# Kernel tuning notes

Measured on AMD Instinct MI355X. Metric: run time of the kernel, lower is better.

## Reference

```python
import jax, jax.numpy as jnp
import numpy as np

PLP_ORDER = 16
N_CHANNEL = 40
FFT_LENGTH = 512
SAMPLE_RATE = 16000
LIFTER = 22
COMP_FACTOR = 0.33
FLOOR = 1e-5
F_MIN = 0.0
F_MAX = SAMPLE_RATE / 2


def _hz_to_mel(hz):
    return 1127.0 * np.log1p(np.asarray(hz, dtype=np.float64) / 700.0)


def _mel_to_hz(mel):
    return 700.0 * np.expm1(np.asarray(mel, dtype=np.float64) / 1127.0)


def _build_constants():
    # SPTK-style mel filter bank (triangular in mel domain).
    mel_min = _hz_to_mel(F_MIN)
    mel_max = _hz_to_mel(F_MAX)
    lower_bin = max(1, int(F_MIN / SAMPLE_RATE * FFT_LENGTH + 1.5))
    upper_bin = min(FFT_LENGTH // 2, int(F_MAX / SAMPLE_RATE * FFT_LENGTH + 0.5))
    seed = np.arange(1, N_CHANNEL + 2)
    cf_mel = (mel_max - mel_min) / (N_CHANNEL + 1) * seed + mel_min  # (C+1,)
    bins = np.arange(lower_bin, upper_bin)
    mel = _hz_to_mel(SAMPLE_RATE * bins / FFT_LENGTH)
    ch = np.searchsorted(cf_mel, mel, side='left')  # first center freq >= mel
    diff = cf_mel - np.concatenate([[mel_min], cf_mel[:-1]])
    w = (cf_mel[ch] - mel) / diff[ch]
    H = np.zeros((len(bins), N_CHANNEL))
    rows = np.arange(len(bins))
    low = ch - 1
    m_lo = low >= 0
    H[rows[m_lo], low[m_lo]] += w[m_lo]
    m_hi = ch <= N_CHANNEL - 1
    H[rows[m_hi], ch[m_hi]] += 1.0 - w[m_hi]
    # Equal-loudness curve over the first C center frequencies (in Hz).
    cf_hz = _mel_to_hz(cf_mel)
    f2 = cf_hz[:N_CHANNEL] ** 2
    eql = (f2 / (f2 + 160000.0)) ** 2 * (f2 + 1440000.0) / (f2 + 9610000.0)
    # Liftering vector, v[0] = 2.
    m = np.arange(PLP_ORDER + 1)
    lift = 1.0 + LIFTER / 2.0 * np.sin(np.pi / LIFTER * m)
    lift[0] = 2.0
    return lower_bin, upper_bin, H.astype(np.float32), eql.astype(np.float32), lift.astype(np.float32)


LOWER_BIN, UPPER_BIN, H_NP, EQL_NP, LIFT_NP = _build_constants()


def _levinson_durbin(r):
    # r: (..., M+1) autocorrelation -> (gain K, LPC coefficients a_1..a_M)
    M = PLP_ORDER
    E = r[..., 0]
    a = jnp.zeros(r.shape[:-1] + (M,), r.dtype)
    for i in range(1, M + 1):
        acc = r[..., i]
        if i > 1:
            acc = acc + jnp.einsum('...j,...j->...', a[..., : i - 1], r[..., 1:i][..., ::-1])
        k = -acc / E
        if i > 1:
            a = a.at[..., : i - 1].set(a[..., : i - 1] + k[..., None] * a[..., : i - 1][..., ::-1])
        a = a.at[..., i - 1].set(k)
        E = E * (1.0 - k * k)
    return jnp.sqrt(E), a


def _lpc_to_cepstrum(K, a):
    # c0 = log K; c_m = -a_m - sum_{k=1}^{m-1} (k/m) c_k a_{m-k}
    M = PLP_ORDER
    c = [jnp.log(K)]
    for m in range(1, M + 1):
        acc = a[..., m - 1]
        for k in range(1, m):
            acc = acc + (k / m) * c[k] * a[..., m - k - 1]
        c.append(-acc)
    return jnp.stack(c, axis=-1)  # (..., M+1)


def _plp(x):
    H = jnp.asarray(H_NP)
    eql = jnp.asarray(EQL_NP)
    lift = jnp.asarray(LIFT_NP)
    # Mel filter bank on power spectrum (use_power=True)
    fb = jnp.matmul(x[..., LOWER_BIN:UPPER_BIN], H)          # (..., C)
    logfb = jnp.log(jnp.maximum(fb, FLOOR))
    # Equal-loudness scaling + cubic-root amplitude compression
    y = (jnp.exp(logfb) * eql) ** COMP_FACTOR                # (..., C)
    # replicate1: duplicate first and last channels
    y = jnp.concatenate([y[..., :1], y, y[..., -1:]], axis=-1)  # (..., C+2)
    n = y.shape[-1]
    # hfft with norm='forward' -> inverse-FFT-like autocorrelation
    r = jnp.fft.hfft(y) / (2 * (n - 1))
    r = r[..., : PLP_ORDER + 1]
    K, a = _levinson_durbin(r)
    c = _lpc_to_cepstrum(K, a)
    c = c * lift
    return c[..., 1:]  # out_format 'y': PLP without C0, (..., M)


def setup_inputs() -> dict:
    key = jax.random.key(0)
    x = jax.random.uniform(key, (32, 4096, FFT_LENGTH // 2 + 1), dtype=jnp.float32)
    return {"x": x}


def reference(x):
    return _plp(x)
```

## Files before the change

### kernel.cpp

```cpp
#include <hip/hip_runtime.h>
#include <cmath>

#define NBINS 257
#define NCH   40
#define MORD  16
#define NR    17
#define NY    42
#define CHUNK 16
#define FPB   64

__global__ __launch_bounds__(256) void plp_kernel(const float* __restrict__ x,
                                                  float* __restrict__ out,
                                                  int nframes)
{
    __shared__ float xs[CHUNK][257];
    __shared__ float ys[CHUNK][NY + 1];
    __shared__ float rs[FPB][NR];
    __shared__ float ttab[256];
    __shared__ int   sstart[NCH + 2];
    __shared__ float eql_s[NCH];
    __shared__ float lift_s[NR];
    __shared__ float ct[NR][NY + 1];

    const int tid = threadIdx.x;
    const double PI = 3.14159265358979323846;

    const double MELMAX = 1127.0 * log1p(8000.0 / 700.0);
    const double U = MELMAX / 41.0;
    if (tid < 255) {
        int b = tid + 1;
        double mel = 1127.0 * log1p((31.25 * (double)b) / 700.0);
        ttab[b] = (float)(mel / U);
    }
    if (tid < NCH + 2) {
        double thr = 22.4 * expm1(((double)tid * U) / 1127.0);
        int s = (int)floor(thr) + 1;
        s = s < 1 ? 1 : (s > 256 ? 256 : s);
        sstart[tid] = s;
    }
    if (tid < NCH) {
        double cf = 700.0 * expm1(((double)(tid + 1) * U) / 1127.0);
        double f2 = cf * cf;
        double e  = f2 / (f2 + 160000.0);
        e = e * e * (f2 + 1440000.0) / (f2 + 9610000.0);
        eql_s[tid] = (float)e;
    }
    if (tid < NR) {
        lift_s[tid] = (float)(1.0 + 11.0 * sin(PI * (double)tid / 22.0));
    }
    for (int idx = tid; idx < NR * NY; idx += 256) {
        int l = idx / NY, j = idx % NY;
        double s = (j == 0 || j == NY - 1) ? 1.0 : 2.0;
        ct[l][j] = (float)(s * cos(PI * (double)(j * l) / 41.0) / 82.0);
    }
    __syncthreads();

    const long long frame0 = (long long)blockIdx.x * FPB;

    for (int chk = 0; chk < FPB / CHUNK; ++chk) {
        const long long cf0 = frame0 + (long long)chk * CHUNK;

        #pragma unroll
        for (int i = 0; i < CHUNK; ++i) {
            long long fr = cf0 + i;
            if (fr > (long long)nframes - 1) fr = (long long)nframes - 1;
            xs[i][tid] = x[fr * NBINS + 1 + tid];
        }
        __syncthreads();

        for (int task = tid; task < CHUNK * NCH; task += 256) {
            int f = task / NCH, c = task % NCH;
            int s0 = sstart[c], s1 = sstart[c + 1], s2 = sstart[c + 2];
            float acc = 0.f;
            for (int b = s0; b < s1; ++b) acc = fmaf(ttab[b] - (float)c, xs[f][b - 1], acc);
            for (int b = s1; b < s2; ++b) acc = fmaf((float)(c + 2) - ttab[b], xs[f][b - 1], acc);
            float v  = fmaxf(acc, 1e-5f) * eql_s[c];
            float yv = powf(v, 0.33f);
            ys[f][c + 1] = yv;
            if (c == 0)       ys[f][0]      = yv;
            if (c == NCH - 1) ys[f][NY - 1] = yv;
        }
        __syncthreads();

        for (int task = tid; task < CHUNK * NR; task += 256) {
            int f = task / NR, l = task % NR;
            float acc = 0.f;
            #pragma unroll
            for (int j = 0; j < NY; ++j) acc = fmaf(ct[l][j], ys[f][j], acc);
            rs[chk * CHUNK + f][l] = acc;
        }
        __syncthreads();
    }

    if (tid < FPB && frame0 + tid < (long long)nframes) {
        float r[NR];
        #pragma unroll
        for (int i = 0; i < NR; ++i) r[i] = rs[tid][i];

        float a[MORD];
        #pragma unroll
        for (int i = 0; i < MORD; ++i) a[i] = 0.f;
        float E = r[0];
        #pragma unroll
        for (int i = 1; i <= MORD; ++i) {
            float acc = r[i];
            #pragma unroll
            for (int j = 0; j < i - 1; ++j) acc = fmaf(a[j], r[i - 1 - j], acc);
            float k = -acc / E;
            const int half = (i - 1) / 2;
            #pragma unroll
            for (int j = 0; j < half; ++j) {
                float t1 = a[j], t2 = a[i - 2 - j];
                a[j]         = fmaf(k, t2, t1);
                a[i - 2 - j] = fmaf(k, t1, t2);
            }
            if ((i - 1) & 1) {
                a[half] = fmaf(k, a[half], a[half]);
            }
            a[i - 1] = k;
            E = E * (1.f - k * k);
        }

        float cc[NR];
        #pragma unroll
        for (int m = 1; m <= MORD; ++m) {
            float acc = a[m - 1];
            #pragma unroll
            for (int k2 = 1; k2 < m; ++k2)
                acc = fmaf(((float)k2 / (float)m) * cc[k2], a[m - k2 - 1], acc);
            cc[m] = -acc;
        }

        float o[16];
        #pragma unroll
        for (int m = 1; m <= MORD; ++m) o[m - 1] = cc[m] * lift_s[m];

        float4* op = reinterpret_cast<float4*>(out + (size_t)(frame0 + tid) * 16);
        op[0] = make_float4(o[0],  o[1],  o[2],  o[3]);
        op[1] = make_float4(o[4],  o[5],  o[6],  o[7]);
        op[2] = make_float4(o[8],  o[9],  o[10], o[11]);
        op[3] = make_float4(o[12], o[13], o[14], o[15]);
    }
}

extern "C" void kernel_launch(void* const* d_in, const int* in_sizes, int n_in,
                              void* d_out, int out_size, void* d_ws, size_t ws_size,
                              hipStream_t stream) {
    const float* x  = (const float*)d_in[0];
    float*      outp = (float*)d_out;
    int nframes = in_sizes[0] / NBINS;
    int nblocks = (nframes + FPB - 1) / FPB;
    plp_kernel<<<nblocks, 256, 0, stream>>>(x, outp, nframes);
}
```

Baseline: 239.7 us.

## Compute each frame entirely per thread with compile-time constant tables

Replaces the block-cooperative shared-memory pipeline with a one-thread-per-frame kernel. All filterbank weights, DCT cosines, equal-loudness and lifter tables are computed at compile time via constexpr, so they become immediates and the per-block table setup and barriers disappear. powf is swapped for fast exp/log intrinsics. The risk is uncoalesced strided global loads, since each thread reads its own 257-float row, plus heavy register pressure from the fully unrolled per-thread state.

```diff
diff --git a/kernel.cpp b/kernel.cpp
--- a/kernel.cpp
+++ b/kernel.cpp
@@ -1,154 +1,180 @@
 #include <hip/hip_runtime.h>
-#include <cmath>
 
-#define NBINS 257
 #define NCH   40
 #define MORD  16
 #define NR    17
 #define NY    42
-#define CHUNK 16
-#define FPB   64
+#define NBINS 257
+
+namespace cfg {
+
+constexpr double PI  = 3.14159265358979323846264338327950288;
+constexpr double LN2 = 0.693147180559945309417232121458176568;
+
+constexpr double cexp(double x) {
+    double t = 1.0, s = 1.0;
+    for (int i = 1; i < 40; ++i) { t *= x / i; s += t; }
+    return s;
+}
+
+constexpr double clog(double z) {
+    double lg = 0.0;
+    while (z > 1.4142135623730951) { z *= 0.5; lg += LN2; }
+    while (z < 0.7071067811865476) { z *= 2.0; lg -= LN2; }
+    double u = (z - 1.0) / (z + 1.0), u2 = u * u, t = u, s = u;
+    for (int k = 1; k < 24; ++k) { t *= u2; s += t / (2.0 * k + 1.0); }
+    return lg + 2.0 * s;
+}
+
+constexpr double ccos(double x) {
+    double tp = 2.0 * PI;
+    double q = x / tp;
+    long long k = (long long)(q + (q >= 0.0 ? 0.5 : -0.5));
+    double r = x - (double)k * tp;
+    double r2 = r * r, t = 1.0, s = 1.0;
+    for (int i = 1; i < 20; ++i) { t *= -r2 / ((2.0 * i - 1.0) * (2.0 * i)); s += t; }
+    return s;
+}
+
+constexpr double csin(double x) { return ccos(x - PI / 2.0); }
+
+struct Tab {
+    int   start[43];
+    float w[257];
+    float eql[NCH];
+    float lift[NR];
+    float ct[NR][NY];
+    constexpr Tab() : start(), w(), eql(), lift(), ct() {
+        const double lmax  = clog(87.0 / 7.0);
+        const double U1127 = lmax / 41.0;
+        for (int c = 0; c <= 42 - 1; ++c) {
+            double thr = 22.4 * (cexp((double)c * U1127) - 1.0);
+            int s = (int)thr + 1;
+            if (s < 1) s = 1;
+            if (s > 256) s = 256;
+            start[c] = s;
+        }
+        start[42 - 1] = start[41];
+        for (int c = 0; c <= 40; ++c) {
+            for (int b = start[c]; b < start[c + 1]; ++b) {
+                double mel = 1127.0 * clog(1.0 + (double)b * 31.25 / 700.0);
+                double t   = mel / (1127.0 * U1127);
+                w[b] = (float)(t - (double)c);
+            }
+        }
+        for (int c = 0; c < NCH; ++c) {
+            double cf = 700.0 * (cexp((double)(c + 1) * U1127) - 1.0);
+            double f2 = cf * cf;
+            double e  = f2 / (f2 + 160000.0);
+            e = e * e * (f2 + 1440000.0) / (f2 + 9610000.0);
+            eql[c] = (float)e;
+        }
+        for (int m = 0; m < NR; ++m)
+            lift[m] = (float)(1.0 + 11.0 * csin(PI * (double)m / 22.0));
+        lift[0] = 2.0f;
+        for (int l = 0; l < NR; ++l)
+            for (int j = 0; j < NY; ++j) {
+                double s = (j == 0 || j == NY - 1) ? 1.0 : 2.0;
+                ct[l][j] = (float)(s * ccos(PI * (double)(j * l) / 41.0) / 82.0);
+            }
+    }
+};
+
+constexpr Tab T{};
+
+}
 
 __global__ __launch_bounds__(256) void plp_kernel(const float* __restrict__ x,
                                                   float* __restrict__ out,
                                                   int nframes)
 {
-    __shared__ float xs[CHUNK][257];
-    __shared__ float ys[CHUNK][NY + 1];
-    __shared__ float rs[FPB][NR];
-    __shared__ float ttab[256];
-    __shared__ int   sstart[NCH + 2];
-    __shared__ float eql_s[NCH];
-    __shared__ float lift_s[NR];
-    __shared__ float ct[NR][NY + 1];
+    using cfg::T;
+    const long long frame = (long long)blockIdx.x * blockDim.x + threadIdx.x;
+    if (frame >= nframes) return;
+    const float* __restrict__ xf = x + frame * NBINS;
 
-    const int tid = threadIdx.x;
-    const double PI = 3.14159265358979323846;
+    float fb[NCH];
+    #pragma unroll
+    for (int c = 0; c < NCH; ++c) fb[c] = 0.f;
 
-    const double MELMAX = 1127.0 * log1p(8000.0 / 700.0);
-    const double U = MELMAX / 41.0;
-    if (tid < 255) {
-        int b = tid + 1;
-        double mel = 1127.0 * log1p((31.25 * (double)b) / 700.0);
-        ttab[b] = (float)(mel / U);
-    }
-    if (tid < NCH + 2) {
-        double thr = 22.4 * expm1(((double)tid * U) / 1127.0);
-        int s = (int)floor(thr) + 1;
-        s = s < 1 ? 1 : (s > 256 ? 256 : s);
-        sstart[tid] = s;
-    }
-    if (tid < NCH) {
-        double cf = 700.0 * expm1(((double)(tid + 1) * U) / 1127.0);
-        double f2 = cf * cf;
-        double e  = f2 / (f2 + 160000.0);
-        e = e * e * (f2 + 1440000.0) / (f2 + 9610000.0);
-        eql_s[tid] = (float)e;
-    }
-    if (tid < NR) {
-        lift_s[tid] = (float)(1.0 + 11.0 * sin(PI * (double)tid / 22.0));
-    }
-    for (int idx = tid; idx < NR * NY; idx += 256) {
-        int l = idx / NY, j = idx % NY;
-        double s = (j == 0 || j == NY - 1) ? 1.0 : 2.0;
-        ct[l][j] = (float)(s * cos(PI * (double)(j * l) / 41.0) / 82.0);
-    }
-    __syncthreads();
-
-    const long long frame0 = (long long)blockIdx.x * FPB;
-
-    for (int chk = 0; chk < FPB / CHUNK; ++chk) {
-        const long long cf0 = frame0 + (long long)chk * CHUNK;
-
+    #pragma unroll
+    for (int c = 0; c <= 40; ++c) {
         #pragma unroll
-        for (int i = 0; i < CHUNK; ++i) {
-            long long fr = cf0 + i;
-            if (fr > (long long)nframes - 1) fr = (long long)nframes - 1;
-            xs[i][tid] = x[fr * NBINS + 1 + tid];
+        for (int b = T.start[c]; b < T.start[c + 1]; ++b) {
+            float xv = xf[b];
+            const float wa = T.w[b];
+            if (c < 40) fb[c]     = fmaf(wa, xv, fb[c]);
+            if (c >= 1) fb[c - 1] = fmaf(1.0f - wa, xv, fb[c - 1]);
         }
-        __syncthreads();
-
-        for (int task = tid; task < CHUNK * NCH; task += 256) {
-            int f = task / NCH, c = task % NCH;
-            int s0 = sstart[c], s1 = sstart[c + 1], s2 = sstart[c + 2];
-            float acc = 0.f;
-            for (int b = s0; b < s1; ++b) acc = fmaf(ttab[b] - (float)c, xs[f][b - 1], acc);
-            for (int b = s1; b < s2; ++b) acc = fmaf((float)(c + 2) - ttab[b], xs[f][b - 1], acc);
-            float v  = fmaxf(acc, 1e-5f) * eql_s[c];
-            float yv = powf(v, 0.33f);
-            ys[f][c + 1] = yv;
-            if (c == 0)       ys[f][0]      = yv;
-            if (c == NCH - 1) ys[f][NY - 1] = yv;
-        }
-        __syncthreads();
-
-        for (int task = tid; task < CHUNK * NR; task += 256) {
-            int f = task / NR, l = task % NR;
-            float acc = 0.f;
-            #pragma unroll
-            for (int j = 0; j < NY; ++j) acc = fmaf(ct[l][j], ys[f][j], acc);
-            rs[chk * CHUNK + f][l] = acc;
-        }
-        __syncthreads();
     }
 
-    if (tid < FPB && frame0 + tid < (long long)nframes) {
-        float r[NR];
+    float ys[NY];
+    #pragma unroll
+    for (int c = 0; c < NCH; ++c) {
+        float v = fmaxf(fb[c], 1e-5f) * T.eql[c];
+        ys[c + 1] = __expf(0.33f * __logf(v));
+    }
+    ys[0] = ys[1];
+    ys[NY - 1] = ys[NY - 2];
+
+    float r[NR];
+    #pragma unroll
+    for (int l = 0; l < NR; ++l) {
+        float acc = 0.f;
         #pragma unroll
-        for (int i = 0; i < NR; ++i) r[i] = rs[tid][i];
+        for (int j = 0; j < NY; ++j) acc = fmaf(T.ct[l][j], ys[j], acc);
+        r[l] = acc;
+    }
 
-        float a[MORD];
+    float a[MORD];
+    #pragma unroll
+    for (int i = 0; i < MORD; ++i) a[i] = 0.f;
+    float E = r[0];
+    #pragma unroll
+    for (int i = 1; i <= MORD; ++i) {
+        float acc = r[i];
         #pragma unroll
-        for (int i = 0; i < MORD; ++i) a[i] = 0.f;
-        float E = r[0];
+        for (int j = 0; j < i - 1; ++j) acc = fmaf(a[j], r[i - 1 - j], acc);
+        float k = -acc / E;
+        const int half = (i - 1) / 2;
         #pragma unroll
-        for (int i = 1; i <= MORD; ++i) {
-            float acc = r[i];
-            #pragma unroll
-            for (int j = 0; j < i - 1; ++j) acc = fmaf(a[j], r[i - 1 - j], acc);
-            float k = -acc / E;
-            const int half = (i - 1) / 2;
-            #pragma unroll
-            for (int j = 0; j < half; ++j) {
-                float t1 = a[j], t2 = a[i - 2 - j];
-                a[j]         = fmaf(k, t2, t1);
-                a[i - 2 - j] = fmaf(k, t1, t2);
-            }
-            if ((i - 1) & 1) {
-                a[half] = fmaf(k, a[half], a[half]);
-            }
-            a[i - 1] = k;
-            E = E * (1.f - k * k);
+        for (int j = 0; j < half; ++j) {
+            float t1 = a[j], t2 = a[i - 2 - j];
+            a[j]         = fmaf(k, t2, t1);
+            a[i - 2 - j] = fmaf(k, t1, t2);
         }
+        if ((i - 1) & 1) a[half] = fmaf(k, a[half], a[half]);
+        a[i - 1] = k;
+        E = E * (1.f - k * k);
+    }
 
-        float cc[NR];
+    float cc[NR];
+    #pragma unroll
+    for (int m = 1; m <= MORD; ++m) {
+        float acc = a[m - 1];
         #pragma unroll
-        for (int m = 1; m <= MORD; ++m) {
-            float acc = a[m - 1];
-            #pragma unroll
-            for (int k2 = 1; k2 < m; ++k2)
-                acc = fmaf(((float)k2 / (float)m) * cc[k2], a[m - k2 - 1], acc);
-            cc[m] = -acc;
-        }
+        for (int k2 = 1; k2 < m; ++k2)
+            acc = fmaf(((float)k2 / (float)m) * cc[k2], a[m - k2 - 1], acc);
+        cc[m] = -acc;
+    }
 
-        float o[16];
-        #pragma unroll
-        for (int m = 1; m <= MORD; ++m) o[m - 1] = cc[m] * lift_s[m];
+    float o[16];
+    #pragma unroll
+    for (int m = 1; m <= MORD; ++m) o[m - 1] = cc[m] * T.lift[m];
 
-        float4* op = reinterpret_cast<float4*>(out + (size_t)(frame0 + tid) * 16);
-        op[0] = make_float4(o[0],  o[1],  o[2],  o[3]);
-        op[1] = make_float4(o[4],  o[5],  o[6],  o[7]);
-        op[2] = make_float4(o[8],  o[9],  o[10], o[11]);
-        op[3] = make_float4(o[12], o[13], o[14], o[15]);
-    }
+    float4* op = reinterpret_cast<float4*>(out + (size_t)frame * 16);
+    op[0] = make_float4(o[0],  o[1],  o[2],  o[3]);
+    op[1] = make_float4(o[4],  o[5],  o[6],  o[7]);
+    op[2] = make_float4(o[8],  o[9],  o[10], o[11]);
+    op[3] = make_float4(o[12], o[13], o[14], o[15]);
 }
 
 extern "C" void kernel_launch(void* const* d_in, const int* in_sizes, int n_in,
                               void* d_out, int out_size, void* d_ws, size_t ws_size,
                               hipStream_t stream) {
-    const float* x  = (const float*)d_in[0];
+    const float* x   = (const float*)d_in[0];
     float*      outp = (float*)d_out;
     int nframes = in_sizes[0] / NBINS;
-    int nblocks = (nframes + FPB - 1) / FPB;
+    int nblocks = (nframes + 255) / 256;
     plp_kernel<<<nblocks, 256, 0, stream>>>(x, outp, nframes);
 }
```

New measurement: 221.3 us. 7.7% less time.
